# Kernel optimization log

Measured on AMD Instinct MI355X. Metric: run time of the kernel, lower is better.

## Reference

```python
import jax, jax.numpy as jnp
import numpy as np

EMB_DIM = 384
HEAD_DIM = 64
B, T = 512, 256


def setup_inputs() -> dict:
    key = jax.random.key(0)
    k1, k2, k3, k4 = jax.random.split(key, 4)
    inputs = jax.random.normal(k1, (B, T, EMB_DIM), dtype=jnp.float32)
    # torch nn.Linear weight layout: [out_features, in_features]
    s = EMB_DIM ** -0.5
    WQ = jax.random.normal(k2, (HEAD_DIM, EMB_DIM), dtype=jnp.float32) * s
    WK = jax.random.normal(k3, (HEAD_DIM, EMB_DIM), dtype=jnp.float32) * s
    WV = jax.random.normal(k4, (HEAD_DIM, EMB_DIM), dtype=jnp.float32) * s
    return {"inputs": inputs, "WQ": WQ, "WK": WK, "WV": WV}


def reference(inputs, WQ, WK, WV):
    # Linear (no bias): x @ W.T
    q = jnp.einsum('btc,dc->btd', inputs, WQ)  # [B,T,D]
    k = jnp.einsum('btc,dc->btd', inputs, WK)
    v = jnp.einsum('btc,dc->btd', inputs, WV)
    scale = k.shape[-1] ** -0.5
    scores = jnp.einsum('bqd,bkd->bqk', q, k) * scale  # [B,T,T]
    Tq = inputs.shape[1]
    causal = jnp.tril(jnp.ones((Tq, Tq), dtype=bool))
    scores = jnp.where(causal, scores, -jnp.inf)
    weights = jax.nn.softmax(scores, axis=-1)
    # dropout omitted (eval mode) for a deterministic reference
    out = jnp.einsum('bqk,bkd->bqd', weights, v)  # [B,T,D]
    return out
```

## Files before the change

kernel.cpp:

```cpp
#include <hip/hip_runtime.h>


typedef short s16x8 __attribute__((ext_vector_type(8)));
typedef float f32x4 __attribute__((ext_vector_type(4)));
typedef float f32x2 __attribute__((ext_vector_type(2)));
typedef unsigned int u32;
typedef unsigned int u32x4 __attribute__((ext_vector_type(4)));
typedef unsigned short u16;
typedef unsigned short u16x4 __attribute__((ext_vector_type(4)));
typedef __bf16 bf16x2 __attribute__((ext_vector_type(2)));

__device__ __forceinline__ u32 cvt2(float x, float y) {
  f32x2 v = {x, y};
  bf16x2 b = __builtin_convertvector(v, bf16x2);
  return __builtin_bit_cast(u32, b);
}
__device__ __forceinline__ u16 f2bf(float f) {
  __bf16 b = (__bf16)f;
  return __builtin_bit_cast(u16, b);
}
__device__ __forceinline__ s16x8 pack8(float4 a, float4 b) {
  u32x4 p = {cvt2(a.x, a.y), cvt2(a.z, a.w), cvt2(b.x, b.y), cvt2(b.z, b.w)};
  return __builtin_bit_cast(s16x8, p);
}
__device__ __forceinline__ s16x8 mk_qf(f32x4 a, f32x4 b) {
  u32x4 p = {cvt2(a[0], a[1]), cvt2(a[2], a[3]), cvt2(b[0], b[1]), cvt2(b[2], b[3])};
  return __builtin_bit_cast(s16x8, p);
}

#define MFMA16 __builtin_amdgcn_mfma_f32_16x16x32_bf16

#define VTOF 32768
#define POFF 65536

__global__ __launch_bounds__(1024) void head_kernel(
    const float* __restrict__ x,
    const float* __restrict__ WQ, const float* __restrict__ WK,
    const float* __restrict__ WV, float* __restrict__ out)
{
  __shared__ char smem[147456];
  const int tid = threadIdx.x;
  const int l  = tid & 63;
  const int w  = tid >> 6;
  const int g  = l >> 4, li = l & 15;
  const long bbase = (long)blockIdx.x * 256;

  const int myrow = 16 * w + li;
  const float* px = x + (bbase + myrow) * 384 + g * 8;

  float4 a0 = *reinterpret_cast<const float4*>(px);
  float4 a1 = *reinterpret_cast<const float4*>(px + 4);
  float4 b0 = *reinterpret_cast<const float4*>(px + 32);
  float4 b1 = *reinterpret_cast<const float4*>(px + 36);

#pragma unroll 3
  for (int i = 0; i < 9; ++i) {
    int id = tid + 1024 * i;
    int row = id / 48, slot = id - row * 48;
    const float* wsrc = (row < 64) ? (WQ + row * 384)
                       : (row < 128) ? (WK + (row - 64) * 384)
                                     : (WV + (row - 128) * 384);
    float4 wa = *reinterpret_cast<const float4*>(wsrc + slot * 8);
    float4 wb = *reinterpret_cast<const float4*>(wsrc + slot * 8 + 4);
    *reinterpret_cast<s16x8*>(smem + row * 768 + ((slot ^ (row & 7)) << 4)) =
        pack8(wa, wb);
  }
  __syncthreads();

  f32x4 acc[12];
#pragma unroll
  for (int nt = 0; nt < 12; ++nt) acc[nt] = (f32x4){0.f, 0.f, 0.f, 0.f};

#pragma unroll 1
  for (int t = 0; t < 12; t += 2) {
    s16x8 xfA = pack8(a0, a1);
    if (t + 2 < 12) {
      a0 = *reinterpret_cast<const float4*>(px + (t + 2) * 32);
      a1 = *reinterpret_cast<const float4*>(px + (t + 2) * 32 + 4);
    }
#pragma unroll
    for (int nt = 0; nt < 12; ++nt) {
      const int rw = nt * 16 + li;
      s16x8 af = *reinterpret_cast<const s16x8*>(
          smem + rw * 768 + (((t * 4 + g) ^ (li & 7)) << 4));
      acc[nt] = MFMA16(af, xfA, acc[nt], 0, 0, 0);
    }
    s16x8 xfB = pack8(b0, b1);
    if (t + 3 < 12) {
      b0 = *reinterpret_cast<const float4*>(px + (t + 3) * 32);
      b1 = *reinterpret_cast<const float4*>(px + (t + 3) * 32 + 4);
    }
#pragma unroll
    for (int nt = 0; nt < 12; ++nt) {
      const int rw = nt * 16 + li;
      s16x8 af = *reinterpret_cast<const s16x8*>(
          smem + rw * 768 + ((((t + 1) * 4 + g) ^ (li & 7)) << 4));
      acc[nt] = MFMA16(af, xfB, acc[nt], 0, 0, 0);
    }
  }
  __syncthreads();

  s16x8 qf0 = mk_qf(acc[0], acc[1]);
  s16x8 qf1 = mk_qf(acc[2], acc[3]);
#pragma unroll
  for (int mm = 0; mm < 4; ++mm) {
    const int Eb = 32 * (mm >> 1) + 8 * g + 4 * (mm & 1);
    u16x4 pk;
    pk[0] = f2bf(acc[4 + mm][0]); pk[1] = f2bf(acc[4 + mm][1]);
    pk[2] = f2bf(acc[4 + mm][2]); pk[3] = f2bf(acc[4 + mm][3]);
    *reinterpret_cast<u16x4*>(smem + myrow * 128 +
        (((Eb >> 3) ^ (myrow & 7)) << 4) + (Eb & 7) * 2) = pk;
  }
#pragma unroll
  for (int mm = 0; mm < 4; ++mm)
#pragma unroll
    for (int r = 0; r < 4; ++r) {
      const int d = mm * 16 + 4 * g + r;
      *reinterpret_cast<u16*>(smem + VTOF + d * 512 +
          ((myrow * 2) ^ ((d & 7) << 4))) = f2bf(acc[8 + mm][r]);
    }
  __syncthreads();

  char* Pw = smem + POFF + w * 2048;
  const int qt = w;

  f32x4 o[4];
  float m[4], lsum[4];
#pragma unroll
  for (int r = 0; r < 4; ++r) { m[r] = -1e30f; lsum[r] = 0.f; }
#pragma unroll
  for (int nd = 0; nd < 4; ++nd) o[nd] = (f32x4){0.f, 0.f, 0.f, 0.f};

  const int nc = (qt >> 2) + 1;
#pragma unroll 1
  for (int c = 0; c < nc; ++c) {
    f32x4 s[4];
#pragma unroll
    for (int nj = 0; nj < 4; ++nj) s[nj] = (f32x4){0.f, 0.f, 0.f, 0.f};
#pragma unroll
    for (int nj = 0; nj < 4; ++nj) {
      const int rb = c * 64 + nj * 16 + li;
      s16x8 kf0 = *reinterpret_cast<const s16x8*>(
          smem + rb * 128 + (((0 + g) ^ (rb & 7)) << 4));
      s16x8 kf1 = *reinterpret_cast<const s16x8*>(
          smem + rb * 128 + (((4 + g) ^ (rb & 7)) << 4));
      s[nj] = MFMA16(qf0, kf0, s[nj], 0, 0, 0);
      s[nj] = MFMA16(qf1, kf1, s[nj], 0, 0, 0);
    }
    const bool last = (c == nc - 1);
#pragma unroll
    for (int nj = 0; nj < 4; ++nj)
#pragma unroll
      for (int r = 0; r < 4; ++r) {
        float v = s[nj][r] * 0.125f;
        if (last && (c * 64 + nj * 16 + li) > (qt * 16 + g * 4 + r)) v = -1e30f;
        s[nj][r] = v;
      }
    float alpha[4];
#pragma unroll
    for (int r = 0; r < 4; ++r) {
      float pm = fmaxf(fmaxf(s[0][r], s[1][r]), fmaxf(s[2][r], s[3][r]));
      pm = fmaxf(pm, __shfl_xor(pm, 1));
      pm = fmaxf(pm, __shfl_xor(pm, 2));
      pm = fmaxf(pm, __shfl_xor(pm, 4));
      pm = fmaxf(pm, __shfl_xor(pm, 8));
      float mn = fmaxf(m[r], pm);
      alpha[r] = __expf(m[r] - mn);
      m[r] = mn;
    }
    float psum[4] = {0.f, 0.f, 0.f, 0.f};
#pragma unroll
    for (int nj = 0; nj < 4; ++nj)
#pragma unroll
      for (int r = 0; r < 4; ++r) {
        float p = __expf(s[nj][r] - m[r]);
        psum[r] += p;
        int rowp = g * 4 + r;
        *reinterpret_cast<u16*>(
            Pw + rowp * 128 + ((nj * 32 + li * 2) ^ ((rowp & 7) << 4))) = f2bf(p);
      }
#pragma unroll
    for (int r = 0; r < 4; ++r) {
      float ps = psum[r];
      ps += __shfl_xor(ps, 1);
      ps += __shfl_xor(ps, 2);
      ps += __shfl_xor(ps, 4);
      ps += __shfl_xor(ps, 8);
      lsum[r] = lsum[r] * alpha[r] + ps;
    }
#pragma unroll
    for (int nd = 0; nd < 4; ++nd)
#pragma unroll
      for (int r = 0; r < 4; ++r) o[nd][r] *= alpha[r];

    __asm__ volatile("s_waitcnt lgkmcnt(0)" ::: "memory");
    s16x8 pa[2];
#pragma unroll
    for (int kk = 0; kk < 2; ++kk)
      pa[kk] = *reinterpret_cast<const s16x8*>(
          Pw + li * 128 + (((kk * 4 + g) ^ (li & 7)) << 4));
#pragma unroll
    for (int nd = 0; nd < 4; ++nd) {
#pragma unroll
      for (int kk = 0; kk < 2; ++kk) {
        const int d = nd * 16 + li;
        s16x8 vf = *reinterpret_cast<const s16x8*>(
            smem + VTOF + d * 512 + ((c * 128 + kk * 64 + g * 16) ^ ((d & 7) << 4)));
        o[nd] = MFMA16(pa[kk], vf, o[nd], 0, 0, 0);
      }
    }
  }
#pragma unroll
  for (int r = 0; r < 4; ++r) lsum[r] = 1.f / lsum[r];
#pragma unroll
  for (int nd = 0; nd < 4; ++nd)
#pragma unroll
    for (int r = 0; r < 4; ++r)
      out[(bbase + qt * 16 + g * 4 + r) * 64 + nd * 16 + li] = o[nd][r] * lsum[r];
}

extern "C" void kernel_launch(void* const* d_in, const int* in_sizes, int n_in,
                              void* d_out, int out_size, void* d_ws, size_t ws_size,
                              hipStream_t stream) {
  const float* x  = (const float*)d_in[0];
  const float* WQ = (const float*)d_in[1];
  const float* WK = (const float*)d_in[2];
  const float* WV = (const float*)d_in[3];
  float* out = (float*)d_out;

  head_kernel<<<dim3(512), dim3(1024), 0, stream>>>(x, WQ, WK, WV, out);
}
```

Measured before the change: 63.74 us.

## Stream weight chunks through small LDS buffer and use 32-wide attention chunks

Stops staging all three projection weight matrices in LDS up front and streams one 32-column chunk per K-step through a 12KB buffer, so shared memory drops from 144KB to 80KB. The launch bound now requests more resident blocks per CU. The cost is two barriers per projection step and serialized global weight loads inside the loop. Attention now processes 32 keys per chunk instead of 64, which skips more masked work on the causal diagonal but adds more loop iterations and online-softmax rescales.

```diff
diff --git a/kernel.cpp b/kernel.cpp
--- a/kernel.cpp
+++ b/kernel.cpp
@@ -31,14 +31,14 @@
 #define MFMA16 __builtin_amdgcn_mfma_f32_16x16x32_bf16
 
 #define VTOF 32768
-#define POFF 65536
-
-__global__ __launch_bounds__(1024) void head_kernel(
+#define WCO  65536
+
+__global__ __launch_bounds__(1024, 8) void head_kernel(
     const float* __restrict__ x,
     const float* __restrict__ WQ, const float* __restrict__ WK,
     const float* __restrict__ WV, float* __restrict__ out)
 {
-  __shared__ char smem[147456];
+  __shared__ char smem[81920];
   const int tid = threadIdx.x;
   const int l  = tid & 63;
   const int w  = tid >> 6;
@@ -48,21 +48,23 @@
   const int myrow = 16 * w + li;
   const float* px = x + (bbase + myrow) * 384 + g * 8;
 
+  const int wrow = tid >> 2, wslot = tid & 3;
+  const bool doW = (tid < 768);
+  const float* wrp = nullptr;
+  if (doW)
+    wrp = ((wrow < 64) ? (WQ + wrow * 384)
+          : (wrow < 128) ? (WK + (wrow - 64) * 384)
+                         : (WV + (wrow - 128) * 384)) + wslot * 8;
+  const int wsz = (wrow >> 1) & 3;
+  const int rsz = (li >> 1) & 3;
+
   float4 a0 = *reinterpret_cast<const float4*>(px);
   float4 a1 = *reinterpret_cast<const float4*>(px + 4);
-  float4 b0 = *reinterpret_cast<const float4*>(px + 32);
-  float4 b1 = *reinterpret_cast<const float4*>(px + 36);
-
-#pragma unroll 3
-  for (int i = 0; i < 9; ++i) {
-    int id = tid + 1024 * i;
-    int row = id / 48, slot = id - row * 48;
-    const float* wsrc = (row < 64) ? (WQ + row * 384)
-                       : (row < 128) ? (WK + (row - 64) * 384)
-                                     : (WV + (row - 128) * 384);
-    float4 wa = *reinterpret_cast<const float4*>(wsrc + slot * 8);
-    float4 wb = *reinterpret_cast<const float4*>(wsrc + slot * 8 + 4);
-    *reinterpret_cast<s16x8*>(smem + row * 768 + ((slot ^ (row & 7)) << 4)) =
+
+  if (doW) {
+    float4 wa = *reinterpret_cast<const float4*>(wrp);
+    float4 wb = *reinterpret_cast<const float4*>(wrp + 4);
+    *reinterpret_cast<s16x8*>(smem + WCO + wrow * 64 + ((wslot ^ wsz) << 4)) =
         pack8(wa, wb);
   }
   __syncthreads();
@@ -72,33 +74,27 @@
   for (int nt = 0; nt < 12; ++nt) acc[nt] = (f32x4){0.f, 0.f, 0.f, 0.f};
 
 #pragma unroll 1
-  for (int t = 0; t < 12; t += 2) {
-    s16x8 xfA = pack8(a0, a1);
-    if (t + 2 < 12) {
-      a0 = *reinterpret_cast<const float4*>(px + (t + 2) * 32);
-      a1 = *reinterpret_cast<const float4*>(px + (t + 2) * 32 + 4);
+  for (int t = 0; t < 12; ++t) {
+    s16x8 xf = pack8(a0, a1);
+    if (t < 11) {
+      a0 = *reinterpret_cast<const float4*>(px + (t + 1) * 32);
+      a1 = *reinterpret_cast<const float4*>(px + (t + 1) * 32 + 4);
     }
 #pragma unroll
     for (int nt = 0; nt < 12; ++nt) {
-      const int rw = nt * 16 + li;
       s16x8 af = *reinterpret_cast<const s16x8*>(
-          smem + rw * 768 + (((t * 4 + g) ^ (li & 7)) << 4));
-      acc[nt] = MFMA16(af, xfA, acc[nt], 0, 0, 0);
-    }
-    s16x8 xfB = pack8(b0, b1);
-    if (t + 3 < 12) {
-      b0 = *reinterpret_cast<const float4*>(px + (t + 3) * 32);
-      b1 = *reinterpret_cast<const float4*>(px + (t + 3) * 32 + 4);
-    }
-#pragma unroll
-    for (int nt = 0; nt < 12; ++nt) {
-      const int rw = nt * 16 + li;
-      s16x8 af = *reinterpret_cast<const s16x8*>(
-          smem + rw * 768 + ((((t + 1) * 4 + g) ^ (li & 7)) << 4));
-      acc[nt] = MFMA16(af, xfB, acc[nt], 0, 0, 0);
-    }
-  }
-  __syncthreads();
+          smem + WCO + (nt * 16 + li) * 64 + ((g ^ rsz) << 4));
+      acc[nt] = MFMA16(af, xf, acc[nt], 0, 0, 0);
+    }
+    __syncthreads();
+    if (t < 11 && doW) {
+      float4 wa = *reinterpret_cast<const float4*>(wrp + (t + 1) * 32);
+      float4 wb = *reinterpret_cast<const float4*>(wrp + (t + 1) * 32 + 4);
+      *reinterpret_cast<s16x8*>(smem + WCO + wrow * 64 + ((wslot ^ wsz) << 4)) =
+          pack8(wa, wb);
+    }
+    __syncthreads();
+  }
 
   s16x8 qf0 = mk_qf(acc[0], acc[1]);
   s16x8 qf1 = mk_qf(acc[2], acc[3]);
@@ -121,72 +117,72 @@
     }
   __syncthreads();
 
-  char* Pw = smem + POFF + w * 2048;
+  char* Pw = smem + WCO + w * 1024;
   const int qt = w;
 
   f32x4 o[4];
-  float m[4], lsum[4];
-#pragma unroll
-  for (int r = 0; r < 4; ++r) { m[r] = -1e30f; lsum[r] = 0.f; }
+  float mx[4], ls[4];
+#pragma unroll
+  for (int r = 0; r < 4; ++r) { mx[r] = -1e30f; ls[r] = 0.f; }
 #pragma unroll
   for (int nd = 0; nd < 4; ++nd) o[nd] = (f32x4){0.f, 0.f, 0.f, 0.f};
 
-  const int nc = (qt >> 2) + 1;
+  const int nc = (qt >> 1) + 1;
 #pragma unroll 1
   for (int c = 0; c < nc; ++c) {
-    f32x4 s[4];
-#pragma unroll
-    for (int nj = 0; nj < 4; ++nj) s[nj] = (f32x4){0.f, 0.f, 0.f, 0.f};
-#pragma unroll
-    for (int nj = 0; nj < 4; ++nj) {
-      const int rb = c * 64 + nj * 16 + li;
-      s16x8 kf0 = *reinterpret_cast<const s16x8*>(
-          smem + rb * 128 + (((0 + g) ^ (rb & 7)) << 4));
-      s16x8 kf1 = *reinterpret_cast<const s16x8*>(
-          smem + rb * 128 + (((4 + g) ^ (rb & 7)) << 4));
-      s[nj] = MFMA16(qf0, kf0, s[nj], 0, 0, 0);
-      s[nj] = MFMA16(qf1, kf1, s[nj], 0, 0, 0);
-    }
+    f32x4 s0 = {0.f, 0.f, 0.f, 0.f}, s1 = {0.f, 0.f, 0.f, 0.f};
+    const int rb0 = c * 32 + li, rb1 = rb0 + 16;
+    s16x8 k00 = *reinterpret_cast<const s16x8*>(
+        smem + rb0 * 128 + (((0 + g) ^ (rb0 & 7)) << 4));
+    s16x8 k01 = *reinterpret_cast<const s16x8*>(
+        smem + rb0 * 128 + (((4 + g) ^ (rb0 & 7)) << 4));
+    s16x8 k10 = *reinterpret_cast<const s16x8*>(
+        smem + rb1 * 128 + (((0 + g) ^ (rb1 & 7)) << 4));
+    s16x8 k11 = *reinterpret_cast<const s16x8*>(
+        smem + rb1 * 128 + (((4 + g) ^ (rb1 & 7)) << 4));
+    s0 = MFMA16(qf0, k00, s0, 0, 0, 0);
+    s0 = MFMA16(qf1, k01, s0, 0, 0, 0);
+    s1 = MFMA16(qf0, k10, s1, 0, 0, 0);
+    s1 = MFMA16(qf1, k11, s1, 0, 0, 0);
+
     const bool last = (c == nc - 1);
-#pragma unroll
-    for (int nj = 0; nj < 4; ++nj)
-#pragma unroll
-      for (int r = 0; r < 4; ++r) {
-        float v = s[nj][r] * 0.125f;
-        if (last && (c * 64 + nj * 16 + li) > (qt * 16 + g * 4 + r)) v = -1e30f;
-        s[nj][r] = v;
+    float alpha[4];
+#pragma unroll
+    for (int r = 0; r < 4; ++r) {
+      float v0 = s0[r] * 0.125f, v1 = s1[r] * 0.125f;
+      if (last) {
+        const int qrow = qt * 16 + 4 * g + r;
+        if (c * 32 + li > qrow) v0 = -1e30f;
+        if (c * 32 + 16 + li > qrow) v1 = -1e30f;
       }
-    float alpha[4];
-#pragma unroll
-    for (int r = 0; r < 4; ++r) {
-      float pm = fmaxf(fmaxf(s[0][r], s[1][r]), fmaxf(s[2][r], s[3][r]));
+      s0[r] = v0; s1[r] = v1;
+      float pm = fmaxf(v0, v1);
       pm = fmaxf(pm, __shfl_xor(pm, 1));
       pm = fmaxf(pm, __shfl_xor(pm, 2));
       pm = fmaxf(pm, __shfl_xor(pm, 4));
       pm = fmaxf(pm, __shfl_xor(pm, 8));
-      float mn = fmaxf(m[r], pm);
-      alpha[r] = __expf(m[r] - mn);
-      m[r] = mn;
-    }
-    float psum[4] = {0.f, 0.f, 0.f, 0.f};
-#pragma unroll
-    for (int nj = 0; nj < 4; ++nj)
-#pragma unroll
-      for (int r = 0; r < 4; ++r) {
-        float p = __expf(s[nj][r] - m[r]);
-        psum[r] += p;
-        int rowp = g * 4 + r;
-        *reinterpret_cast<u16*>(
-            Pw + rowp * 128 + ((nj * 32 + li * 2) ^ ((rowp & 7) << 4))) = f2bf(p);
-      }
-#pragma unroll
-    for (int r = 0; r < 4; ++r) {
-      float ps = psum[r];
-      ps += __shfl_xor(ps, 1);
-      ps += __shfl_xor(ps, 2);
-      ps += __shfl_xor(ps, 4);
-      ps += __shfl_xor(ps, 8);
-      lsum[r] = lsum[r] * alpha[r] + ps;
+      const float mn = fmaxf(mx[r], pm);
+      alpha[r] = __expf(mx[r] - mn);
+      mx[r] = mn;
+    }
+    float ps[4];
+#pragma unroll
+    for (int r = 0; r < 4; ++r) {
+      const float p0 = __expf(s0[r] - mx[r]);
+      const float p1 = __expf(s1[r] - mx[r]);
+      ps[r] = p0 + p1;
+      const int rp = 4 * g + r;
+      *reinterpret_cast<u16*>(Pw + rp * 64 + li * 2) = f2bf(p0);
+      *reinterpret_cast<u16*>(Pw + rp * 64 + 32 + li * 2) = f2bf(p1);
+    }
+#pragma unroll
+    for (int r = 0; r < 4; ++r) {
+      float t = ps[r];
+      t += __shfl_xor(t, 1);
+      t += __shfl_xor(t, 2);
+      t += __shfl_xor(t, 4);
+      t += __shfl_xor(t, 8);
+      ls[r] = ls[r] * alpha[r] + t;
     }
 #pragma unroll
     for (int nd = 0; nd < 4; ++nd)
@@ -194,29 +190,22 @@
       for (int r = 0; r < 4; ++r) o[nd][r] *= alpha[r];
 
     __asm__ volatile("s_waitcnt lgkmcnt(0)" ::: "memory");
-    s16x8 pa[2];
-#pragma unroll
-    for (int kk = 0; kk < 2; ++kk)
-      pa[kk] = *reinterpret_cast<const s16x8*>(
-          Pw + li * 128 + (((kk * 4 + g) ^ (li & 7)) << 4));
+    s16x8 pa = *reinterpret_cast<const s16x8*>(Pw + li * 64 + g * 16);
 #pragma unroll
     for (int nd = 0; nd < 4; ++nd) {
-#pragma unroll
-      for (int kk = 0; kk < 2; ++kk) {
-        const int d = nd * 16 + li;
-        s16x8 vf = *reinterpret_cast<const s16x8*>(
-            smem + VTOF + d * 512 + ((c * 128 + kk * 64 + g * 16) ^ ((d & 7) << 4)));
-        o[nd] = MFMA16(pa[kk], vf, o[nd], 0, 0, 0);
-      }
-    }
-  }
-#pragma unroll
-  for (int r = 0; r < 4; ++r) lsum[r] = 1.f / lsum[r];
+      const int d = nd * 16 + li;
+      s16x8 vf = *reinterpret_cast<const s16x8*>(
+          smem + VTOF + d * 512 + ((c * 64 + g * 16) ^ ((d & 7) << 4)));
+      o[nd] = MFMA16(pa, vf, o[nd], 0, 0, 0);
+    }
+  }
+#pragma unroll
+  for (int r = 0; r < 4; ++r) ls[r] = 1.f / ls[r];
 #pragma unroll
   for (int nd = 0; nd < 4; ++nd)
 #pragma unroll
     for (int r = 0; r < 4; ++r)
-      out[(bbase + qt * 16 + g * 4 + r) * 64 + nd * 16 + li] = o[nd][r] * lsum[r];
+      out[(bbase + qt * 16 + 4 * g + r) * 64 + nd * 16 + li] = o[nd][r] * ls[r];
 }
 
 extern "C" void kernel_launch(void* const* d_in, const int* in_sizes, int n_in,
```

Measured after the change: 145.3 us. +128.0%, slower.
